# Performance work log

Hardware: AMD Instinct MI355X
Metric: run time of the kernel (lower is better)

Reference implementation:

```python
import jax, jax.numpy as jnp
import numpy as np

V, E, HID, T, S = 50000, 512, 1024, 32, 4096
H = HID // 2  # per-direction hidden size


def setup_inputs() -> dict:
    key = jax.random.key(0)
    ks = jax.random.split(key, 16)
    f = lambda k, shape, s=0.1: (jax.random.normal(k, shape) * s).astype(jnp.float32)
    return {
        "input_ids": jax.random.randint(ks[0], (S,), 0, V),
        "target": jax.random.randint(ks[1], (S,), 0, T),
        "emb": f(ks[2], (V, E)),
        "wih_f": f(ks[3], (4 * H, E)),
        "whh_f": f(ks[4], (4 * H, H)),
        "b_f": f(ks[5], (4 * H,)),
        "wih_b": f(ks[6], (4 * H, E)),
        "whh_b": f(ks[7], (4 * H, H)),
        "b_b": f(ks[8], (4 * H,)),
        "lin_w": f(ks[9], (T, HID)),
        "lin_b": f(ks[10], (T,)),
        "start_trans": f(ks[11], (T,)),
        "end_trans": f(ks[12], (T,)),
        "trans": f(ks[13], (T, T)),
    }


def _lstm_dir(xp, whh):
    # xp: [S, 4H] precomputed input projections (x @ Wih^T + b_ih + b_hh)
    Hh = whh.shape[1]

    def step(carry, x_t):
        h, c = carry
        gates = x_t + whh @ h  # [4H]; PyTorch gate order: i, f, g, o
        i, fg, g, o = jnp.split(gates, 4)
        i = jax.nn.sigmoid(i)
        fg = jax.nn.sigmoid(fg)
        g = jnp.tanh(g)
        o = jax.nn.sigmoid(o)
        c = fg * c + i * g
        h = o * jnp.tanh(c)
        return (h, c), h

    init = (jnp.zeros((Hh,), xp.dtype), jnp.zeros((Hh,), xp.dtype))
    _, hs = jax.lax.scan(step, init, xp)
    return hs  # [S, H]


def reference(input_ids, target, emb, wih_f, whh_f, b_f, wih_b, whh_b, b_b,
              lin_w, lin_b, start_trans, end_trans, trans):
    x = emb[input_ids]  # [S, E]
    # bidirectional LSTM (batch of 1 sequence); dropout is identity (eval mode)
    h_f = _lstm_dir(x @ wih_f.T + b_f, whh_f)                # [S, H]
    h_b = _lstm_dir((x[::-1]) @ wih_b.T + b_b, whh_b)[::-1]  # [S, H]
    lstm_out = jnp.concatenate([h_f, h_b], axis=-1)          # [S, HID]
    em = lstm_out @ lin_w.T + lin_b                          # [S, T] emissions

    # CRF negative log-likelihood (mask all ones, batch=1, reduction='sum')
    idx = jnp.arange(em.shape[0])
    score = (start_trans[target[0]]
             + jnp.sum(em[idx, target])
             + jnp.sum(trans[target[:-1], target[1:]])
             + end_trans[target[-1]])

    alpha0 = start_trans + em[0]  # [T]

    def fstep(alpha, e_t):
        # logsumexp over previous tag: [T,1] + [T,T] -> [T]
        alpha = jax.scipy.special.logsumexp(alpha[:, None] + trans, axis=0) + e_t
        return alpha, None

    alpha, _ = jax.lax.scan(fstep, alpha0, em[1:])
    logZ = jax.scipy.special.logsumexp(alpha + end_trans)
    return logZ - score  # -log p(target | input), scalar
```

## Files before the change

kernel.cpp:

```cpp
#include <hip/hip_runtime.h>
#include <hip/hip_bf16.h>

#define S_LEN 4096
#define HID   512
#define E_DIM 512
#define G4    2048

__device__ __forceinline__ unsigned int f2b(float f) {
  unsigned int x = __float_as_uint(f);
  return (x + 0x7FFFu + ((x >> 16) & 1u)) >> 16;
}
__device__ __forceinline__ float b2f(unsigned int b) {
  return __uint_as_float(b << 16);
}

__global__ __launch_bounds__(256) void proj_gemm(
    const int* __restrict__ ids, const float* __restrict__ emb,
    const float* __restrict__ wih_f, const float* __restrict__ wih_b,
    const float* __restrict__ b_f, const float* __restrict__ b_b,
    float* __restrict__ xp_f, float* __restrict__ xp_b)
{
  const int dir = blockIdx.z;
  const float* __restrict__ wih  = dir ? wih_b : wih_f;
  const float* __restrict__ bias = dir ? b_b : b_f;
  float* __restrict__ out = dir ? xp_b : xp_f;
  const int i0 = blockIdx.y * 128;
  const int j0 = blockIdx.x * 128;
  __shared__ __align__(16) float As[16 * 132];
  __shared__ __align__(16) float Bs[16 * 132];
  const int tid = threadIdx.x;
  const int ti = tid >> 4, tj = tid & 15;

  const int r0 = tid >> 2,        k40 = tid & 3;
  const int r1 = (tid + 256) >> 2, k41 = (tid + 256) & 3;
  const int id0 = ids[dir ? (S_LEN - 1 - (i0 + r0)) : (i0 + r0)];
  const int id1 = ids[dir ? (S_LEN - 1 - (i0 + r1)) : (i0 + r1)];
  const float* a0p = emb + (size_t)id0 * E_DIM + k40 * 4;
  const float* a1p = emb + (size_t)id1 * E_DIM + k41 * 4;
  const float* b0p = wih + (size_t)(j0 + r0) * E_DIM + k40 * 4;
  const float* b1p = wih + (size_t)(j0 + r1) * E_DIM + k41 * 4;

  float acc[8][8];
  #pragma unroll
  for (int x = 0; x < 8; ++x)
    #pragma unroll
    for (int y = 0; y < 8; ++y) acc[x][y] = 0.f;

  for (int k0 = 0; k0 < E_DIM; k0 += 16) {
    float4 va0 = *(const float4*)(a0p + k0);
    float4 va1 = *(const float4*)(a1p + k0);
    float4 vb0 = *(const float4*)(b0p + k0);
    float4 vb1 = *(const float4*)(b1p + k0);
    As[(k40*4+0)*132 + r0] = va0.x; As[(k40*4+1)*132 + r0] = va0.y;
    As[(k40*4+2)*132 + r0] = va0.z; As[(k40*4+3)*132 + r0] = va0.w;
    As[(k41*4+0)*132 + r1] = va1.x; As[(k41*4+1)*132 + r1] = va1.y;
    As[(k41*4+2)*132 + r1] = va1.z; As[(k41*4+3)*132 + r1] = va1.w;
    Bs[(k40*4+0)*132 + r0] = vb0.x; Bs[(k40*4+1)*132 + r0] = vb0.y;
    Bs[(k40*4+2)*132 + r0] = vb0.z; Bs[(k40*4+3)*132 + r0] = vb0.w;
    Bs[(k41*4+0)*132 + r1] = vb1.x; Bs[(k41*4+1)*132 + r1] = vb1.y;
    Bs[(k41*4+2)*132 + r1] = vb1.z; Bs[(k41*4+3)*132 + r1] = vb1.w;
    __syncthreads();
    const float4* As4 = (const float4*)As;
    const float4* Bs4 = (const float4*)Bs;
    #pragma unroll
    for (int k = 0; k < 16; ++k) {
      float4 al = As4[k*33 + ti];
      float4 ah = As4[k*33 + 16 + ti];
      float4 bl = Bs4[k*33 + tj];
      float4 bh = Bs4[k*33 + 16 + tj];
      float a[8] = {al.x, al.y, al.z, al.w, ah.x, ah.y, ah.z, ah.w};
      float b[8] = {bl.x, bl.y, bl.z, bl.w, bh.x, bh.y, bh.z, bh.w};
      #pragma unroll
      for (int x = 0; x < 8; ++x)
        #pragma unroll
        for (int y = 0; y < 8; ++y) acc[x][y] = fmaf(a[x], b[y], acc[x][y]);
    }
    __syncthreads();
  }
  float4 blo = *(const float4*)(bias + j0 + tj * 4);
  float4 bhi = *(const float4*)(bias + j0 + 64 + tj * 4);
  #pragma unroll
  for (int x = 0; x < 8; ++x) {
    int gi = i0 + ((x < 4) ? (ti * 4 + x) : (64 + ti * 4 + (x - 4)));
    float* orow = out + (size_t)gi * G4 + j0;
    float4 o0 = make_float4(acc[x][0] + blo.x, acc[x][1] + blo.y,
                            acc[x][2] + blo.z, acc[x][3] + blo.w);
    float4 o1 = make_float4(acc[x][4] + bhi.x, acc[x][5] + bhi.y,
                            acc[x][6] + bhi.z, acc[x][7] + bhi.w);
    *(float4*)(orow + tj * 4) = o0;
    *(float4*)(orow + 64 + tj * 4) = o1;
  }
}

__global__ __launch_bounds__(512, 2) void lstm_rec(
    const float* __restrict__ xp_f, const float* __restrict__ xp_b,
    const float* __restrict__ whh_f, const float* __restrict__ whh_b,
    float* __restrict__ hs, unsigned int* __restrict__ hslot)
{
  const int wg  = blockIdx.x;
  const int dir = wg >> 4, g = wg & 15;
  const float* __restrict__ xp  = dir ? xp_b  : xp_f;
  const float* __restrict__ whh = dir ? whh_b : whh_f;
  unsigned int* slot = hslot + dir * (4 * HID);
  const int tid  = threadIdx.x;
  const int lane = tid & 63;
  const int u_l  = tid >> 4;
  const int gate = (tid >> 2) & 3;
  const int p    = tid & 3;
  const int U0   = g * 32;
  const int grow = gate * 512 + U0 + u_l;
  const bool isg = (gate == 2);
  const bool master = ((tid & 15) == 0);

  float w[128];
  {
    const float4* wp = (const float4*)(whh + (size_t)grow * HID + p * 128);
    #pragma unroll
    for (int u = 0; u < 32; ++u) {
      float4 v = wp[u];
      w[4*u] = v.x; w[4*u+1] = v.y; w[4*u+2] = v.z; w[4*u+3] = v.w;
    }
  }
  __shared__ __align__(16) float h_lds[2][544];
  const int pollpos = (tid >> 7) * 136 + (tid & 127);
  const int ownunit = U0 + u_l;
  const int ownpos  = (ownunit >> 7) * 136 + (ownunit & 127);
  h_lds[0][pollpos] = 0.f;
  __syncthreads();

  float c = 0.f;
  float xpv = xp[grow];
  int buf = 0;
  const unsigned int rel = (unsigned int)(tid - U0);

  for (int t = 0; t < S_LEN; ++t) {
    float a0 = 0.f, a1 = 0.f, a2 = 0.f, a3 = 0.f;
    const float4* hq = (const float4*)(&h_lds[buf][p * 136]);
    #pragma unroll
    for (int u = 0; u < 32; ++u) {
      float4 hv = hq[u];
      a0 = fmaf(w[4*u],   hv.x, a0);
      a1 = fmaf(w[4*u+1], hv.y, a1);
      a2 = fmaf(w[4*u+2], hv.z, a2);
      a3 = fmaf(w[4*u+3], hv.w, a3);
    }
    float acc = (a0 + a1) + (a2 + a3);
    acc += __shfl_xor(acc, 1);
    acc += __shfl_xor(acc, 2);
    float v = acc + xpv;
    if (t + 1 < S_LEN) xpv = xp[(size_t)(t + 1) * G4 + grow];

    float e = __expf(isg ? (v + v) : -v);
    float r = __fdividef(1.f, 1.f + e);
    float act = isg ? (1.f - 2.f * r) : r;
    float a4  = __shfl(act, (lane + 4)  & 63);
    float a8  = __shfl(act, (lane + 8)  & 63);
    float a12 = __shfl(act, (lane + 12) & 63);

    const unsigned int tagn = (unsigned int)(t + 1);
    if (master) {
      float i_ = act, f_ = a4, g_ = a8, o_ = a12;
      c = f_ * c + i_ * g_;
      float e2 = __expf(c + c);
      float th = 1.f - 2.f * __fdividef(1.f, 1.f + e2);
      float h = o_ * th;
      unsigned int hb = f2b(h);
      __hip_atomic_store(&slot[(tagn & 3) * HID + ownunit],
                         (tagn << 16) | hb,
                         __ATOMIC_RELAXED, __HIP_MEMORY_SCOPE_AGENT);
      h_lds[buf ^ 1][ownpos] = b2f(hb);
      const int trow = dir ? (S_LEN - 1 - t) : t;
      hs[(size_t)trow * 1024 + dir * HID + ownunit] = h;
    }
    if (t + 1 < S_LEN) {
      if (rel >= 32u) {
        const unsigned int want = tagn;
        unsigned int* pw = &slot[(tagn & 3) * HID + tid];
        unsigned int vv; int it = 0;
        for (;;) {
          vv = __hip_atomic_load(pw, __ATOMIC_RELAXED, __HIP_MEMORY_SCOPE_AGENT);
          if ((vv >> 16) == want) break;
          if (++it > 64) __builtin_amdgcn_s_sleep(1);
          if (it > (1 << 22)) break;
        }
        h_lds[buf ^ 1][pollpos] = b2f(vv & 0xFFFFu);
      }
      __syncthreads();
    }
    buf ^= 1;
  }
}

__global__ __launch_bounds__(512) void emis_kernel(
    const float* __restrict__ hs, const float* __restrict__ lin_w,
    const float* __restrict__ lin_b, float* __restrict__ em)
{
  __shared__ float4 rows[4096];
  const int t0 = blockIdx.x * 16;
  const int tid = threadIdx.x;
  const float4* hs4 = (const float4*)(hs + (size_t)t0 * 1024);
  #pragma unroll
  for (int it = 0; it < 8; ++it) rows[it * 512 + tid] = hs4[it * 512 + tid];
  __syncthreads();
  const int r = tid >> 5, tag = tid & 31;
  const float4* w4 = (const float4*)(lin_w + (size_t)tag * 1024);
  float acc = 0.f;
  #pragma unroll 4
  for (int k = 0; k < 256; ++k) {
    float4 h = rows[r * 256 + k];
    float4 w = w4[k];
    acc += h.x * w.x + h.y * w.y + h.z * w.z + h.w * w.w;
  }
  em[(size_t)(t0 + r) * 32 + tag] = acc + lin_b[tag];
}

__global__ __launch_bounds__(1024) void crf_pass1(
    const float* __restrict__ em, const float* __restrict__ trans,
    float* __restrict__ Pt)
{
  __shared__ float tr[32 * 33];
  __shared__ float bufA[32 * 33], bufB[32 * 33];
  const int tid = threadIdx.x;
  const int i = tid >> 5, j = tid & 31;
  tr[i * 33 + j] = trans[i * 32 + j];
  const int c = blockIdx.x;
  const int t0 = (c == 0) ? 1 : c * 16;
  const int t1 = c * 16 + 16;
  bufA[i * 33 + j] = trans[i * 32 + j] + em[(size_t)t0 * 32 + j];
  __syncthreads();

  float* cur = bufA;
  float* nxt = bufB;
  for (int t = t0 + 1; t < t1; ++t) {
    float m = -1e30f;
    #pragma unroll
    for (int k = 0; k < 32; ++k)
      m = fmaxf(m, cur[i * 33 + k] + tr[k * 33 + j]);
    float s = 0.f;
    #pragma unroll
    for (int k = 0; k < 32; ++k)
      s += __expf(cur[i * 33 + k] + tr[k * 33 + j] - m);
    float nv = m + __logf(s) + em[(size_t)t * 32 + j];
    nxt[i * 33 + j] = nv;
    __syncthreads();
    float* tmp = cur; cur = nxt; nxt = tmp;
  }
  Pt[(size_t)c * 1024 + tid] = cur[(tid & 31) * 33 + (tid >> 5)];
}

__global__ __launch_bounds__(128) void crf_pass2(
    const float* __restrict__ em, const float* __restrict__ Pt,
    const int* __restrict__ tgt, const float* __restrict__ st,
    const float* __restrict__ et, const float* __restrict__ trans,
    float* __restrict__ out)
{
  __shared__ float als[32];
  __shared__ float gold[2];
  const int tid = threadIdx.x;
  const int lane = tid & 63;
  const int wv = tid >> 6;

  if (wv == 1) {
    float se = 0.f;
    for (int t = lane; t < S_LEN; t += 64) {
      int tg = tgt[t];
      se += em[(size_t)t * 32 + tg];
      if (t + 1 < S_LEN) se += trans[tg * 32 + tgt[t + 1]];
    }
    #pragma unroll
    for (int m = 1; m < 64; m <<= 1) se += __shfl_xor(se, m);
    if (lane == 0) gold[0] = se + st[tgt[0]] + et[tgt[S_LEN - 1]];
  } else {
    const int jj = lane & 31;
    float a = st[jj] + em[jj];
    float4 P0, P1, P2, P3, P4, P5, P6, P7;
    {
      const float* pb = Pt + jj * 32;
      P0 = *(const float4*)(pb +  0); P1 = *(const float4*)(pb +  4);
      P2 = *(const float4*)(pb +  8); P3 = *(const float4*)(pb + 12);
      P4 = *(const float4*)(pb + 16); P5 = *(const float4*)(pb + 20);
      P6 = *(const float4*)(pb + 24); P7 = *(const float4*)(pb + 28);
    }
    for (int cc = 0; cc < 256; ++cc) {
      float4 N0, N1, N2, N3, N4, N5, N6, N7;
      if (cc < 255) {
        const float* pb = Pt + (size_t)(cc + 1) * 1024 + jj * 32;
        N0 = *(const float4*)(pb +  0); N1 = *(const float4*)(pb +  4);
        N2 = *(const float4*)(pb +  8); N3 = *(const float4*)(pb + 12);
        N4 = *(const float4*)(pb + 16); N5 = *(const float4*)(pb + 20);
        N6 = *(const float4*)(pb + 24); N7 = *(const float4*)(pb + 28);
      }
      als[jj] = a;
      float m = -1e30f;
      #define MAXQ(Q, b) \
        m = fmaxf(m, fmaxf(fmaxf(als[b+0] + Q.x, als[b+1] + Q.y), \
                           fmaxf(als[b+2] + Q.z, als[b+3] + Q.w)));
      MAXQ(P0, 0) MAXQ(P1, 4) MAXQ(P2, 8)  MAXQ(P3, 12)
      MAXQ(P4,16) MAXQ(P5,20) MAXQ(P6,24)  MAXQ(P7,28)
      float s = 0.f;
      #define SUMQ(Q, b) \
        s += __expf(als[b+0] + Q.x - m) + __expf(als[b+1] + Q.y - m) + \
             __expf(als[b+2] + Q.z - m) + __expf(als[b+3] + Q.w - m);
      SUMQ(P0, 0) SUMQ(P1, 4) SUMQ(P2, 8)  SUMQ(P3, 12)
      SUMQ(P4,16) SUMQ(P5,20) SUMQ(P6,24)  SUMQ(P7,28)
      #undef MAXQ
      #undef SUMQ
      a = m + __logf(s);
      P0 = N0; P1 = N1; P2 = N2; P3 = N3;
      P4 = N4; P5 = N5; P6 = N6; P7 = N7;
    }
    float x = (lane < 32) ? a + et[jj] : -1e30f;
    float mm = x;
    #pragma unroll
    for (int m2 = 1; m2 < 64; m2 <<= 1) mm = fmaxf(mm, __shfl_xor(mm, m2));
    float ss = (lane < 32) ? __expf(x - mm) : 0.f;
    #pragma unroll
    for (int m2 = 1; m2 < 64; m2 <<= 1) ss += __shfl_xor(ss, m2);
    if (lane == 0) gold[1] = mm + __logf(ss);
  }
  __syncthreads();
  if (tid == 0) out[0] = gold[1] - gold[0];
}

extern "C" void kernel_launch(void* const* d_in, const int* in_sizes, int n_in,
                              void* d_out, int out_size, void* d_ws, size_t ws_size,
                              hipStream_t stream) {
  const int*   ids   = (const int*)d_in[0];
  const int*   tgt   = (const int*)d_in[1];
  const float* emb   = (const float*)d_in[2];
  const float* wih_f = (const float*)d_in[3];
  const float* whh_f = (const float*)d_in[4];
  const float* b_f   = (const float*)d_in[5];
  const float* wih_b = (const float*)d_in[6];
  const float* whh_b = (const float*)d_in[7];
  const float* b_b   = (const float*)d_in[8];
  const float* lin_w = (const float*)d_in[9];
  const float* lin_b = (const float*)d_in[10];
  const float* st    = (const float*)d_in[11];
  const float* et    = (const float*)d_in[12];
  const float* trans = (const float*)d_in[13];

  float* xp_f = (float*)d_ws;
  float* xp_b = xp_f + (size_t)S_LEN * G4;
  float* hs   = xp_b + (size_t)S_LEN * G4;
  float* em   = hs   + (size_t)S_LEN * 1024;
  unsigned int* slot = (unsigned int*)(em + (size_t)S_LEN * 32);
  float* Pt   = xp_f;

  proj_gemm<<<dim3(16, 32, 2), dim3(256), 0, stream>>>(
      ids, emb, wih_f, wih_b, b_f, b_b, xp_f, xp_b);
  lstm_rec<<<dim3(32), dim3(512), 0, stream>>>(
      xp_f, xp_b, whh_f, whh_b, hs, slot);
  emis_kernel<<<dim3(256), dim3(512), 0, stream>>>(hs, lin_w, lin_b, em);
  crf_pass1<<<dim3(256), dim3(1024), 0, stream>>>(em, trans, Pt);
  crf_pass2<<<dim3(1), dim3(128), 0, stream>>>(em, Pt, tgt, st, et, trans,
                                               (float*)d_out);
}
```

Measured before the change: 8.078 ms.

## Restructure LSTM recurrence: per-thread four-gate dot products over packed bf16 hidden state

Each thread now holds a 32-column slice of all four gate rows for its unit, not a 128-column slice of one gate row. It reads the hidden state as packed bf16 pairs from LDS, so each step loads half as many bytes. The 16-lane reduction uses DPP moves for the first two stages and shuffles for the rest, and every lane computes the cell update redundantly. This removes the cross-lane gate gathers and the master-only serial activation tail. The cost is four accumulators, a 16-way reduction per gate, and redundant transcendental math on all lanes.

```diff
diff --git a/kernel.cpp b/kernel.cpp
--- a/kernel.cpp
+++ b/kernel.cpp
@@ -6,12 +6,15 @@
 #define E_DIM 512
 #define G4    2048
 
+__device__ __forceinline__ float fsig(float x) {
+  return __fdividef(1.f, 1.f + __expf(-x));
+}
+__device__ __forceinline__ float ftanh_(float x) {
+  return 1.f - __fdividef(2.f, __expf(2.f * x) + 1.f);
+}
 __device__ __forceinline__ unsigned int f2b(float f) {
   unsigned int x = __float_as_uint(f);
   return (x + 0x7FFFu + ((x >> 16) & 1u)) >> 16;
-}
-__device__ __forceinline__ float b2f(unsigned int b) {
-  return __uint_as_float(b << 16);
 }
 
 __global__ __launch_bounds__(256) void proj_gemm(
@@ -92,6 +95,9 @@
   }
 }
 
+#define DPPADD(a, CTRL) \
+  a += __int_as_float(__builtin_amdgcn_mov_dpp(__float_as_int(a), CTRL, 0xf, 0xf, false));
+
 __global__ __launch_bounds__(512, 2) void lstm_rec(
     const float* __restrict__ xp_f, const float* __restrict__ xp_b,
     const float* __restrict__ whh_f, const float* __restrict__ whh_b,
@@ -102,88 +108,97 @@
   const float* __restrict__ xp  = dir ? xp_b  : xp_f;
   const float* __restrict__ whh = dir ? whh_b : whh_f;
   unsigned int* slot = hslot + dir * (4 * HID);
-  const int tid  = threadIdx.x;
-  const int lane = tid & 63;
-  const int u_l  = tid >> 4;
-  const int gate = (tid >> 2) & 3;
-  const int p    = tid & 3;
-  const int U0   = g * 32;
-  const int grow = gate * 512 + U0 + u_l;
-  const bool isg = (gate == 2);
-  const bool master = ((tid & 15) == 0);
-
-  float w[128];
+  const int tid = threadIdx.x;
+  const int u_l = tid >> 4;
+  const int cs  = tid & 15;
+  const int U0  = g * 32;
+  const int ownunit = U0 + u_l;
+  const bool master = (cs == 0);
+
+  float w0[32], w1[32], w2[32], w3[32];
   {
-    const float4* wp = (const float4*)(whh + (size_t)grow * HID + p * 128);
-    #pragma unroll
-    for (int u = 0; u < 32; ++u) {
-      float4 v = wp[u];
-      w[4*u] = v.x; w[4*u+1] = v.y; w[4*u+2] = v.z; w[4*u+3] = v.w;
-    }
-  }
-  __shared__ __align__(16) float h_lds[2][544];
-  const int pollpos = (tid >> 7) * 136 + (tid & 127);
-  const int ownunit = U0 + u_l;
-  const int ownpos  = (ownunit >> 7) * 136 + (ownunit & 127);
-  h_lds[0][pollpos] = 0.f;
+    const float4* p0 = (const float4*)(whh + (size_t)(0*HID + ownunit) * HID + cs * 32);
+    const float4* p1 = (const float4*)(whh + (size_t)(1*HID + ownunit) * HID + cs * 32);
+    const float4* p2 = (const float4*)(whh + (size_t)(2*HID + ownunit) * HID + cs * 32);
+    const float4* p3 = (const float4*)(whh + (size_t)(3*HID + ownunit) * HID + cs * 32);
+    #pragma unroll
+    for (int q = 0; q < 8; ++q) {
+      float4 a = p0[q]; w0[4*q]=a.x; w0[4*q+1]=a.y; w0[4*q+2]=a.z; w0[4*q+3]=a.w;
+      float4 b = p1[q]; w1[4*q]=b.x; w1[4*q+1]=b.y; w1[4*q+2]=b.z; w1[4*q+3]=b.w;
+      float4 c = p2[q]; w2[4*q]=c.x; w2[4*q+1]=c.y; w2[4*q+2]=c.z; w2[4*q+3]=c.w;
+      float4 d = p3[q]; w3[4*q]=d.x; w3[4*q+1]=d.y; w3[4*q+2]=d.z; w3[4*q+3]=d.w;
+    }
+  }
+
+  __shared__ __align__(16) unsigned int hb_lds[2][320];
+  for (int q = tid; q < 320; q += 512) hb_lds[0][q] = 0u;
   __syncthreads();
 
   float c = 0.f;
-  float xpv = xp[grow];
+  float xpv = (cs < 4) ? xp[(size_t)cs * HID + ownunit] : 0.f;
   int buf = 0;
   const unsigned int rel = (unsigned int)(tid - U0);
 
   for (int t = 0; t < S_LEN; ++t) {
-    float a0 = 0.f, a1 = 0.f, a2 = 0.f, a3 = 0.f;
-    const float4* hq = (const float4*)(&h_lds[buf][p * 136]);
-    #pragma unroll
-    for (int u = 0; u < 32; ++u) {
-      float4 hv = hq[u];
-      a0 = fmaf(w[4*u],   hv.x, a0);
-      a1 = fmaf(w[4*u+1], hv.y, a1);
-      a2 = fmaf(w[4*u+2], hv.z, a2);
-      a3 = fmaf(w[4*u+3], hv.w, a3);
-    }
-    float acc = (a0 + a1) + (a2 + a3);
-    acc += __shfl_xor(acc, 1);
-    acc += __shfl_xor(acc, 2);
-    float v = acc + xpv;
-    if (t + 1 < S_LEN) xpv = xp[(size_t)(t + 1) * G4 + grow];
-
-    float e = __expf(isg ? (v + v) : -v);
-    float r = __fdividef(1.f, 1.f + e);
-    float act = isg ? (1.f - 2.f * r) : r;
-    float a4  = __shfl(act, (lane + 4)  & 63);
-    float a8  = __shfl(act, (lane + 8)  & 63);
-    float a12 = __shfl(act, (lane + 12) & 63);
-
+    const uint4* hq = (const uint4*)(&hb_lds[buf][cs * 20]);
+    uint4 d0 = hq[0], d1 = hq[1], d2 = hq[2], d3 = hq[3];
+    float acc0 = 0.f, acc1 = 0.f, acc2 = 0.f, acc3 = 0.f;
+    #define DW(dw, k) { \
+      float lo = __uint_as_float((dw) << 16); \
+      float hi = __uint_as_float((dw) & 0xffff0000u); \
+      acc0 = fmaf(w0[2*(k)], lo, acc0); acc0 = fmaf(w0[2*(k)+1], hi, acc0); \
+      acc1 = fmaf(w1[2*(k)], lo, acc1); acc1 = fmaf(w1[2*(k)+1], hi, acc1); \
+      acc2 = fmaf(w2[2*(k)], lo, acc2); acc2 = fmaf(w2[2*(k)+1], hi, acc2); \
+      acc3 = fmaf(w3[2*(k)], lo, acc3); acc3 = fmaf(w3[2*(k)+1], hi, acc3); }
+    DW(d0.x, 0)  DW(d0.y, 1)  DW(d0.z, 2)  DW(d0.w, 3)
+    DW(d1.x, 4)  DW(d1.y, 5)  DW(d1.z, 6)  DW(d1.w, 7)
+    DW(d2.x, 8)  DW(d2.y, 9)  DW(d2.z, 10) DW(d2.w, 11)
+    DW(d3.x, 12) DW(d3.y, 13) DW(d3.z, 14) DW(d3.w, 15)
+    #undef DW
+
+    acc0 += (cs == 0) ? xpv : 0.f;
+    acc1 += (cs == 1) ? xpv : 0.f;
+    acc2 += (cs == 2) ? xpv : 0.f;
+    acc3 += (cs == 3) ? xpv : 0.f;
+
+    DPPADD(acc0, 0xB1) DPPADD(acc1, 0xB1) DPPADD(acc2, 0xB1) DPPADD(acc3, 0xB1)
+    DPPADD(acc0, 0x4E) DPPADD(acc1, 0x4E) DPPADD(acc2, 0x4E) DPPADD(acc3, 0x4E)
+    acc0 += __shfl_xor(acc0, 4);  acc1 += __shfl_xor(acc1, 4);
+    acc2 += __shfl_xor(acc2, 4);  acc3 += __shfl_xor(acc3, 4);
+    acc0 += __shfl_xor(acc0, 8);  acc1 += __shfl_xor(acc1, 8);
+    acc2 += __shfl_xor(acc2, 8);  acc3 += __shfl_xor(acc3, 8);
+
+    float i_ = fsig(acc0), f_ = fsig(acc1), g_ = ftanh_(acc2), o_ = fsig(acc3);
+    c = f_ * c + i_ * g_;
+    float h = o_ * ftanh_(c);
+    unsigned int hbits = f2b(h);
     const unsigned int tagn = (unsigned int)(t + 1);
+
     if (master) {
-      float i_ = act, f_ = a4, g_ = a8, o_ = a12;
-      c = f_ * c + i_ * g_;
-      float e2 = __expf(c + c);
-      float th = 1.f - 2.f * __fdividef(1.f, 1.f + e2);
-      float h = o_ * th;
-      unsigned int hb = f2b(h);
       __hip_atomic_store(&slot[(tagn & 3) * HID + ownunit],
-                         (tagn << 16) | hb,
+                         (tagn << 16) | hbits,
                          __ATOMIC_RELAXED, __HIP_MEMORY_SCOPE_AGENT);
-      h_lds[buf ^ 1][ownpos] = b2f(hb);
       const int trow = dir ? (S_LEN - 1 - t) : t;
       hs[(size_t)trow * 1024 + dir * HID + ownunit] = h;
-    }
+      unsigned short* hp = (unsigned short*)&hb_lds[buf ^ 1][0];
+      int d = ownunit >> 1;
+      hp[(((d >> 4) * 20 + (d & 15)) << 1) + (ownunit & 1)] = (unsigned short)hbits;
+    }
+    asm volatile("" ::: "memory");
     if (t + 1 < S_LEN) {
+      if (cs < 4) xpv = xp[(size_t)(t + 1) * G4 + cs * HID + ownunit];
       if (rel >= 32u) {
-        const unsigned int want = tagn;
         unsigned int* pw = &slot[(tagn & 3) * HID + tid];
         unsigned int vv; int it = 0;
         for (;;) {
           vv = __hip_atomic_load(pw, __ATOMIC_RELAXED, __HIP_MEMORY_SCOPE_AGENT);
-          if ((vv >> 16) == want) break;
+          if ((vv >> 16) == tagn) break;
           if (++it > 64) __builtin_amdgcn_s_sleep(1);
-          if (it > (1 << 22)) break;
+          if (it > (1 << 22)) { vv = tagn << 16; break; }
         }
-        h_lds[buf ^ 1][pollpos] = b2f(vv & 0xFFFFu);
+        unsigned short* hp = (unsigned short*)&hb_lds[buf ^ 1][0];
+        int d = tid >> 1;
+        hp[(((d >> 4) * 20 + (d & 15)) << 1) + (tid & 1)] = (unsigned short)(vv & 0xFFFFu);
       }
       __syncthreads();
     }
```

After: 9.026 ms. 1.12x slower.
